# Performance work log

Hardware: AMD Instinct MI355X
Metric: run time of the kernel (lower is better)

## Reference

```python
import jax, jax.numpy as jnp
import numpy as np
from jax import lax

H = 1024
D = 128
T = 64  # n_step + n_middle


def gru_cell(x, h, w_ih, w_hh, b_ih, b_hh):
    # torch.nn.GRUCell gate order: r, z, n
    gi = x @ w_ih.T + b_ih
    gh = h @ w_hh.T + b_hh
    ir, iz, i_n = jnp.split(gi, 3, axis=-1)
    hr, hz, h_n = jnp.split(gh, 3, axis=-1)
    r = jax.nn.sigmoid(ir + hr)
    z = jax.nn.sigmoid(iz + hz)
    n = jnp.tanh(i_n + r * h_n)
    return (1.0 - z) * n + z * h


def decoder(z_seq, z8, n1, w_init, b_init, wi1, wh1, bi1, bh1, wi2, wh2, bi2, bh2, w_out, b_out):
    B = z_seq.shape[0]
    out0 = jnp.zeros((B, D), z_seq.dtype).at[:, -1].set(1.0)
    h0 = z8 @ w_init.T + b_init              # [B, H]
    h1 = jnp.zeros_like(h0)                  # replaced at i == 0
    xs = (jnp.arange(T), jnp.swapaxes(z_seq, 0, 1))  # ([T], [T, B, D])

    def step(carry, x):
        h0, h1, out = carry
        i, z_i = x
        inp = jnp.where(i <= n1 - 1, z_i, out)
        h0n = gru_cell(inp, h0, wi1, wh1, bi1, bh1)
        h1 = jnp.where(i == 0, h0n, h1)
        h1n = gru_cell(h0n, h1, wi2, wh2, bi2, bh2)
        out = h1n @ w_out.T + b_out          # [B, 128]
        return (h0n, h1n, out), out

    _, outs = lax.scan(step, (h0, h1, out0), xs)  # [T, B, 128]
    return jnp.swapaxes(outs[n1 - 1:], 0, 1)      # [B, T-n1+1, 128]


def _p(key, shape):
    return jax.random.normal(key, shape, dtype=jnp.float32) * 0.02


def setup_inputs() -> dict:
    key = jax.random.key(0)
    ks = jax.random.split(key, 32)
    B = 2048
    inp = {
        'zp': jax.random.normal(ks[0], (B, T, D), jnp.float32),
        'zr': jax.random.normal(ks[1], (B, T, D), jnp.float32),
        'zp8': jax.random.normal(ks[2], (B, D), jnp.float32),
        'zr8': jax.random.normal(ks[3], (B, D), jnp.float32),
        'n1': 16,
        'n2': 48,
    }
    # GRU cells 1..4: (w_ih [3H, in], w_hh [3H, H], b_ih [3H], b_hh [3H])
    for j, name in enumerate(['1', '2', '3', '4']):
        in_dim = D if name in ('1', '3') else H
        inp['wi' + name] = _p(ks[4 + 4 * j], (3 * H, in_dim))
        inp['wh' + name] = _p(ks[5 + 4 * j], (3 * H, H))
        inp['bi' + name] = _p(ks[6 + 4 * j], (3 * H,))
        inp['bh' + name] = _p(ks[7 + 4 * j], (3 * H,))
    inp['w_init0'] = _p(ks[20], (H, D)); inp['b_init0'] = _p(ks[21], (H,))
    inp['w_init1'] = _p(ks[22], (H, D)); inp['b_init1'] = _p(ks[23], (H,))
    inp['w_out0'] = _p(ks[24], (D, H)); inp['b_out0'] = _p(ks[25], (D,))
    inp['w_out1'] = _p(ks[26], (D, H)); inp['b_out1'] = _p(ks[27], (D,))
    return inp


def reference(zp, zr, zp8, zr8, n1, n2,
              wi1, wh1, bi1, bh1, wi2, wh2, bi2, bh2,
              wi3, wh3, bi3, bh3, wi4, wh4, bi4, bh4,
              w_init0, b_init0, w_init1, b_init1,
              w_out0, b_out0, w_out1, b_out1):
    z_r = decoder(zr, zr8, n1, w_init0, b_init0, wi1, wh1, bi1, bh1,
                  wi2, wh2, bi2, bh2, w_out0, b_out0)
    z_p = decoder(zp, zp8, n1, w_init1, b_init1, wi3, wh3, bi3, bh3,
                  wi4, wh4, bi4, bh4, w_out1, b_out1)
    return (z_p, z_r)
```

## Files before the change

kernel.cpp:

```cpp
#include <hip/hip_runtime.h>

typedef unsigned short u16;
typedef unsigned int u32;
typedef __attribute__((ext_vector_type(8))) short short8;
typedef __attribute__((ext_vector_type(4))) float f32x4;

#define DEV __device__ __forceinline__
#define SB0() __builtin_amdgcn_sched_barrier(0)

DEV u16 f2bf(float f){
  u32 u = __builtin_bit_cast(u32, f);
  u += 0x7fffu + ((u >> 16) & 1u);
  return (u16)(u >> 16);
}
DEV float sigm(float x){ return 1.f / (1.f + __expf(-x)); }
DEV float tanh_(float x){ return 2.f / (1.f + __expf(-2.f * x)) - 1.f; }

DEV void gl_lds16(const void* g, void* l){
  __builtin_amdgcn_global_load_lds(
      (const __attribute__((address_space(1))) u32*)g,
      (__attribute__((address_space(3))) u32*)l, 16, 0, 0);
}

#define MFMA16(A,B,C) __builtin_amdgcn_mfma_f32_16x16x32_bf16(A, B, C, 0, 0, 0)
#define LGKM0() do{ asm volatile("s_waitcnt lgkmcnt(0)" ::: "memory"); SB0(); }while(0)

__global__ void pack_w_kernel(const float* __restrict__ wi, const float* __restrict__ wh,
                              u16* __restrict__ dst, int Ki, int Kh, int nrows){
  const int KT = Ki + Kh;
  const long n = (long)nrows * KT;
  for (long idx = (long)blockIdx.x * blockDim.x + threadIdx.x; idx < n;
       idx += (long)gridDim.x * blockDim.x){
    int r = (int)(idx / KT), c = (int)(idx % KT);
    float v = (c < Ki) ? wi[(long)r * Ki + c] : wh[(long)r * Kh + (c - Ki)];
    dst[idx] = f2bf(v);
  }
}

struct InitA { const float* z8; const float* wini; const float* bini; float* h0f; u16* h0bf; };

__global__ __launch_bounds__(256)
void init_kernel(InitA A0, InitA A1){
  const InitA& a = (blockIdx.z == 0) ? A0 : A1;
  __shared__ float lz[64][128];
  const int tid = threadIdx.x;
  const int rb = blockIdx.x * 64, ub = blockIdx.y * 128;
  {
    const int row = tid >> 2, q = tid & 3;
    const float4* p = (const float4*)(a.z8 + (long)(rb + row) * 128 + q * 32);
    float4* dst = (float4*)&lz[row][q * 32];
    #pragma unroll
    for (int j = 0; j < 8; ++j) dst[j] = p[j];
  }
  __syncthreads();
  const int u = ub + (tid & 127);
  const int rg = tid >> 7;
  float acc[32];
  #pragma unroll
  for (int r = 0; r < 32; ++r) acc[r] = 0.f;
  for (int k = 0; k < 128; k += 4){
    float4 w4 = *(const float4*)&a.wini[(long)u * 128 + k];
    #pragma unroll
    for (int r = 0; r < 32; ++r){
      float4 z4 = *(const float4*)&lz[rg * 32 + r][k];
      acc[r] += w4.x * z4.x + w4.y * z4.y + w4.z * z4.z + w4.w * z4.w;
    }
  }
  const float b = a.bini[u];
  #pragma unroll
  for (int r = 0; r < 32; ++r){
    const long row = rb + rg * 32 + r;
    const float v = acc[r] + b;
    a.h0f[row * 1024 + u] = v;
    a.h0bf[row * 1024 + u] = f2bf(v);
  }
}

struct CellA {
  const u16* W;
  const float* bi; const float* bh;
  const float* afz; const float* afo;
  const u16* ab1; const u16* ab2;
  const float* holdr; float* holdw; u16* hbfw;
};

template<int CELL>
__global__ __attribute__((amdgpu_waves_per_eu(2, 2))) __launch_bounds__(512)
void cell_kernel(CellA A0, CellA A1, const int* dn1, int step){
  constexpr int KTOT = (CELL == 1) ? 1152 : 2048;
  constexpr int KT = KTOT / 64;
  constexpr int NI_STEPS = (CELL == 1) ? 2 : 16;

  __shared__ u16 lA[2][256 * 64];
  __shared__ u16 lB[2][192 * 64];

  const CellA& a = (blockIdx.y == 0) ? A0 : A1;
  const int tid = threadIdx.x;
  const int lane = tid & 63;
  const int wv = tid >> 6;
  const int wm = wv >> 1;
  const int wn = wv & 1;
  const int bid = blockIdx.x;
  const int inner = bid >> 3;
  const int m_idx = ((bid >> 2) & 1) * 4 + (inner & 3);
  const int n_idx = (bid & 3) * 4 + (inner >> 2);
  const int brow = m_idx * 256;
  const int u0 = n_idx * 64;

  f32x4 aR[4][2] = {}; f32x4 aZ[4][2] = {};
  f32x4 aNI[4][2] = {}; f32x4 aNH[4][2] = {};

  const int srow = tid >> 3;
  const int sxor8 = ((tid & 7) ^ (srow & 7)) * 8;

  auto stage = [&](int bf, int kt){
    const int k0 = kt * 64;
    const u16* ab; int kk;
    if constexpr (CELL == 1){ ab = a.ab1; kk = k0 - 128; }
    else { if (k0 < 1024){ ab = a.ab1; kk = k0; } else { ab = a.ab2; kk = k0 - 1024; } }
    #pragma unroll
    for (int j = 0; j < 4; ++j)
      gl_lds16(ab + (long)(brow + j * 64 + srow) * 1024 + kk + sxor8,
               &lA[bf][(j * 64 + wv * 8) * 64]);
    #pragma unroll
    for (int g = 0; g < 3; ++g)
      gl_lds16(a.W + (long)(g * 1024 + u0 + srow) * KTOT + k0 + sxor8,
               &lB[bf][(g * 64 + wv * 8) * 64]);
  };

  const int l15 = lane & 15;
  const int kq = lane >> 4;
  const int sx = lane & 7;

  auto read_a_ks = [&](int bf, int ks, short8 (&af)[4]){
    const int soff = (((ks * 4 + kq) ^ sx)) * 8;
    #pragma unroll
    for (int fr = 0; fr < 4; ++fr)
      af[fr] = *(const short8*)&lA[bf][(wm * 64 + fr * 16 + l15) * 64 + soff];
  };
  auto read_b_ks = [&](int bf, int g, int ks, short8 (&bg)[2]){
    const int soff = (((ks * 4 + kq) ^ sx)) * 8;
    #pragma unroll
    for (int fc = 0; fc < 2; ++fc)
      bg[fc] = *(const short8*)&lB[bf][(g * 64 + wn * 32 + fc * 16 + l15) * 64 + soff];
  };
  auto mfma8 = [&](const short8 (&af)[4], const short8 (&bg)[2], f32x4 (&A)[4][2]){
    #pragma unroll
    for (int fr = 0; fr < 4; ++fr)
      #pragma unroll
      for (int fc = 0; fc < 2; ++fc)
        A[fr][fc] = MFMA16(af[fr], bg[fc], A[fr][fc]);
  };

  int kstart;
  if constexpr (CELL == 1){
    const int n1v = *dn1;
    const float* fsrc; long fstr;
    if (step < n1v){ fsrc = a.afz; fstr = 64 * 128; }
    else           { fsrc = a.afo; fstr = 128; }
    {
      const int row = tid >> 1, half = tid & 1;
      #pragma unroll
      for (int st = 0; st < 2; ++st){
        const float* pp = fsrc + (long)(brow + row) * fstr + st * 64 + half * 32;
        #pragma unroll
        for (int q = 0; q < 4; ++q){
          float4 x = ((const float4*)pp)[2 * q];
          float4 y = ((const float4*)pp)[2 * q + 1];
          short8 o;
          o[0] = (short)f2bf(x.x); o[1] = (short)f2bf(x.y);
          o[2] = (short)f2bf(x.z); o[3] = (short)f2bf(x.w);
          o[4] = (short)f2bf(y.x); o[5] = (short)f2bf(y.y);
          o[6] = (short)f2bf(y.z); o[7] = (short)f2bf(y.w);
          const int s = half * 4 + q;
          *(short8*)&lA[st][row * 64 + ((s ^ (row & 7)) * 8)] = o;
        }
        #pragma unroll
        for (int g = 0; g < 3; ++g)
          gl_lds16(a.W + (long)(g * 1024 + u0 + srow) * KTOT + st * 64 + sxor8,
                   &lB[st][(g * 64 + wv * 8) * 64]);
      }
    }
    __syncthreads();
    #pragma unroll
    for (int st = 0; st < 2; ++st){
      short8 af0[4], af1[4], b0[2], b1[2];
      read_a_ks(st, 0, af0); read_a_ks(st, 1, af1);
      read_b_ks(st, 0, 0, b0); read_b_ks(st, 0, 1, b1);
      LGKM0();
      mfma8(af0, b0, aR); mfma8(af1, b1, aR);
      read_b_ks(st, 1, 0, b0); read_b_ks(st, 1, 1, b1);
      LGKM0();
      mfma8(af0, b0, aZ); mfma8(af1, b1, aZ);
      read_b_ks(st, 2, 0, b0); read_b_ks(st, 2, 1, b1);
      LGKM0();
      mfma8(af0, b0, aNI); mfma8(af1, b1, aNI);
    }
    __syncthreads();
    stage(0, 2); stage(1, 3);
    asm volatile("s_waitcnt vmcnt(7)" ::: "memory"); SB0();
    __builtin_amdgcn_s_barrier();
    kstart = 2;
  } else {
    stage(0, 0); stage(1, 1);
    asm volatile("s_waitcnt vmcnt(7)" ::: "memory"); SB0();
    __builtin_amdgcn_s_barrier();
    kstart = 0;
  }

  for (int kt = kstart; kt < KT; ++kt){
    const int b = kt & 1;
    short8 af0[4], af1[4], bR0[2], bR1[2], bZ0[2], bZ1[2], bN0[2], bN1[2];
    read_a_ks(b, 0, af0); read_b_ks(b, 0, 0, bR0); read_b_ks(b, 1, 0, bZ0);
    __builtin_amdgcn_s_barrier();
    LGKM0();
    __builtin_amdgcn_s_setprio(1);
    mfma8(af0, bR0, aR);
    __builtin_amdgcn_s_setprio(0);
    __builtin_amdgcn_s_barrier(); SB0();
    read_b_ks(b, 2, 0, bN0); read_a_ks(b, 1, af1);
    __builtin_amdgcn_s_barrier();
    LGKM0();
    __builtin_amdgcn_s_setprio(1);
    mfma8(af0, bZ0, aZ);
    if (kt < NI_STEPS) mfma8(af0, bN0, aNI); else mfma8(af0, bN0, aNH);
    __builtin_amdgcn_s_setprio(0);
    __builtin_amdgcn_s_barrier(); SB0();
    read_b_ks(b, 0, 1, bR1); read_b_ks(b, 1, 1, bZ1); read_b_ks(b, 2, 1, bN1);
    __builtin_amdgcn_s_barrier();
    LGKM0();
    __builtin_amdgcn_s_setprio(1);
    mfma8(af1, bR1, aR);
    __builtin_amdgcn_s_setprio(0);
    __builtin_amdgcn_s_barrier(); SB0();
    if (kt + 2 < KT) stage(b, kt + 2);
    __builtin_amdgcn_s_setprio(1);
    mfma8(af1, bZ1, aZ);
    if (kt < NI_STEPS) mfma8(af1, bN1, aNI); else mfma8(af1, bN1, aNH);
    __builtin_amdgcn_s_setprio(0);
    if (kt < KT - 2)       { asm volatile("s_waitcnt vmcnt(7)" ::: "memory"); SB0(); }
    else if (kt == KT - 2) { asm volatile("s_waitcnt vmcnt(0)" ::: "memory"); SB0(); }
    if (kt + 1 < KT) __builtin_amdgcn_s_barrier();
  }

  const int rq = (lane >> 4) * 4;
  #pragma unroll
  for (int fc = 0; fc < 2; ++fc){
    const int u = u0 + wn * 32 + fc * 16 + l15;
    const float br = a.bi[u] + a.bh[u];
    const float bz = a.bi[1024 + u] + a.bh[1024 + u];
    const float bni = a.bi[2048 + u];
    const float bnh = a.bh[2048 + u];
    #pragma unroll
    for (int fr = 0; fr < 4; ++fr){
      #pragma unroll
      for (int rg = 0; rg < 4; ++rg){
        const long row = brow + wm * 64 + fr * 16 + rq + rg;
        const float r = sigm(aR[fr][fc][rg] + br);
        const float z = sigm(aZ[fr][fc][rg] + bz);
        const float n = tanh_(aNI[fr][fc][rg] + bni + r * (aNH[fr][fc][rg] + bnh));
        const float hp = a.holdr[row * 1024 + u];
        const float hn = (1.f - z) * n + z * hp;
        a.holdw[row * 1024 + u] = hn;
        a.hbfw[row * 1024 + u] = f2bf(hn);
      }
    }
  }
}

struct OutA { const u16* Ah; const u16* Wo; const float* bo; float* outf; };

__global__ __launch_bounds__(256, 2)
void out_kernel(OutA A0, OutA A1, const int* dn1, int step, float* __restrict__ dout, long outhalf){
  const int n1v = *dn1;
  if (step < n1v - 1) return;
  __shared__ u16 lA[2][32 * 64];
  __shared__ u16 lB[2][128 * 64];
  const OutA& a = (blockIdx.y == 0) ? A0 : A1;
  const int tid = threadIdx.x, lane = tid & 63, wv = tid >> 6;
  const int brow = blockIdx.x * 32;
  f32x4 acc[2][2] = {};
  const int srow = tid >> 3;
  const int sxor8 = ((tid & 7) ^ (srow & 7)) * 8;

  auto stage = [&](int bf, int kt){
    const int k0 = kt * 64;
    gl_lds16(a.Ah + (long)(brow + srow) * 1024 + k0 + sxor8, &lA[bf][wv * 8 * 64]);
    #pragma unroll
    for (int j = 0; j < 4; ++j)
      gl_lds16(a.Wo + (long)(j * 32 + srow) * 1024 + k0 + sxor8,
               &lB[bf][(j * 32 + wv * 8) * 64]);
  };

  stage(0, 0); stage(1, 1);
  const int l15 = lane & 15, kq = lane >> 4, sx = lane & 7;
  for (int kt = 0; kt < 16; ++kt){
    const int b = kt & 1;
    if (kt < 15) asm volatile("s_waitcnt vmcnt(5)" ::: "memory");
    else         asm volatile("s_waitcnt vmcnt(0)" ::: "memory");
    SB0();
    __builtin_amdgcn_s_barrier();
    SB0();
    short8 af[2][2], bf2[2][2];
    #pragma unroll
    for (int ks = 0; ks < 2; ++ks){
      const int soff = (((ks * 4 + kq) ^ sx)) * 8;
      af[ks][0] = *(const short8*)&lA[b][(l15) * 64 + soff];
      af[ks][1] = *(const short8*)&lA[b][(16 + l15) * 64 + soff];
      bf2[ks][0] = *(const short8*)&lB[b][(wv * 32 + l15) * 64 + soff];
      bf2[ks][1] = *(const short8*)&lB[b][(wv * 32 + 16 + l15) * 64 + soff];
    }
    asm volatile("s_waitcnt lgkmcnt(0)" ::: "memory"); SB0();
    __builtin_amdgcn_s_barrier();
    SB0();
    if (kt + 2 < 16) stage(b, kt + 2);
    __builtin_amdgcn_s_setprio(1);
    #pragma unroll
    for (int ks = 0; ks < 2; ++ks)
      #pragma unroll
      for (int fr = 0; fr < 2; ++fr)
        #pragma unroll
        for (int fc = 0; fc < 2; ++fc)
          acc[fr][fc] = MFMA16(af[ks][fr], bf2[ks][fc], acc[fr][fc]);
    __builtin_amdgcn_s_setprio(0);
  }
  const int nst = 65 - n1v;
  const int t = step - (n1v - 1);
  const int rq = (lane >> 4) * 4;
  #pragma unroll
  for (int fc = 0; fc < 2; ++fc){
    const int u = wv * 32 + fc * 16 + l15;
    const float bo = a.bo[u];
    #pragma unroll
    for (int fr = 0; fr < 2; ++fr){
      #pragma unroll
      for (int rg = 0; rg < 4; ++rg){
        const long row = brow + fr * 16 + rq + rg;
        const float v = acc[fr][fc][rg] + bo;
        a.outf[row * 128 + u] = v;
        dout[(long)blockIdx.y * outhalf + (row * nst + t) * 128 + u] = v;
      }
    }
  }
}

extern "C" void kernel_launch(void* const* d_in, const int* in_sizes, int n_in,
                              void* d_out, int out_size, void* d_ws, size_t ws_size,
                              hipStream_t stream){
  const float* zz[2]   = { (const float*)d_in[0],  (const float*)d_in[1] };
  const float* z8[2]   = { (const float*)d_in[2],  (const float*)d_in[3] };
  const int* dn1       = (const int*)d_in[4];
  const float* wi_c1[2] = { (const float*)d_in[14], (const float*)d_in[6] };
  const float* wh_c1[2] = { (const float*)d_in[15], (const float*)d_in[7] };
  const float* bi_c1[2] = { (const float*)d_in[16], (const float*)d_in[8] };
  const float* bh_c1[2] = { (const float*)d_in[17], (const float*)d_in[9] };
  const float* wi_c2[2] = { (const float*)d_in[18], (const float*)d_in[10] };
  const float* wh_c2[2] = { (const float*)d_in[19], (const float*)d_in[11] };
  const float* bi_c2[2] = { (const float*)d_in[20], (const float*)d_in[12] };
  const float* bh_c2[2] = { (const float*)d_in[21], (const float*)d_in[13] };
  const float* wini[2]  = { (const float*)d_in[24], (const float*)d_in[22] };
  const float* bini[2]  = { (const float*)d_in[25], (const float*)d_in[23] };
  const float* wout[2]  = { (const float*)d_in[28], (const float*)d_in[26] };
  const float* bout[2]  = { (const float*)d_in[29], (const float*)d_in[27] };

  char* p = (char*)d_ws;
  auto alloc = [&](size_t bytes)->char*{
    char* q = p; p += (bytes + 255) & ~(size_t)255; return q;
  };
  u16* W1c[2]; u16* W2c[2]; u16* Woc[2];
  float* h0f[2]; float* h1f[2]; float* outf[2];
  u16* h0bf[2][2]; u16* h1bf[2][2];
  for (int d = 0; d < 2; ++d){
    W1c[d] = (u16*)alloc(3072ULL * 1152 * 2);
    W2c[d] = (u16*)alloc(3072ULL * 2048 * 2);
    Woc[d] = (u16*)alloc(128ULL * 1024 * 2);
    h0f[d] = (float*)alloc(2048ULL * 1024 * 4);
    h1f[d] = (float*)alloc(2048ULL * 1024 * 4);
    outf[d] = (float*)alloc(2048ULL * 128 * 4);
    for (int b = 0; b < 2; ++b){
      h0bf[d][b] = (u16*)alloc(2048ULL * 1024 * 2);
      h1bf[d][b] = (u16*)alloc(2048ULL * 1024 * 2);
    }
  }
  if ((size_t)(p - (char*)d_ws) > ws_size) return;

  for (int d = 0; d < 2; ++d){
    pack_w_kernel<<<dim3(1024), dim3(256), 0, stream>>>(wi_c1[d], wh_c1[d], W1c[d], 128, 1024, 3072);
    pack_w_kernel<<<dim3(1024), dim3(256), 0, stream>>>(wi_c2[d], wh_c2[d], W2c[d], 1024, 1024, 3072);
    pack_w_kernel<<<dim3(64),   dim3(256), 0, stream>>>(wout[d], wout[d], Woc[d], 1024, 0, 128);
  }
  {
    InitA I0{ z8[0], wini[0], bini[0], h0f[0], h0bf[0][0] };
    InitA I1{ z8[1], wini[1], bini[1], h0f[1], h0bf[1][0] };
    init_kernel<<<dim3(32, 8, 2), dim3(256), 0, stream>>>(I0, I1);
  }

  const long outhalf = (long)out_size / 2;

  for (int i = 0; i < 64; ++i){
    const int cur = i & 1, nxt = cur ^ 1;
    CellA c1[2], c2[2];
    for (int d = 0; d < 2; ++d){
      c1[d] = CellA{ W1c[d], bi_c1[d], bh_c1[d],
                     zz[d] + (long)i * 128, outf[d],
                     h0bf[d][cur], nullptr,
                     h0f[d], h0f[d], h0bf[d][nxt] };
      c2[d] = CellA{ W2c[d], bi_c2[d], bh_c2[d],
                     nullptr, nullptr,
                     h0bf[d][nxt], (i == 0) ? h0bf[d][nxt] : h1bf[d][cur],
                     (i == 0) ? h0f[d] : h1f[d], h1f[d], h1bf[d][nxt] };
    }
    cell_kernel<1><<<dim3(128, 2), dim3(512), 0, stream>>>(c1[0], c1[1], dn1, i);
    cell_kernel<2><<<dim3(128, 2), dim3(512), 0, stream>>>(c2[0], c2[1], dn1, i);
    OutA o0{ h1bf[0][nxt], Woc[0], bout[0], outf[0] };
    OutA o1{ h1bf[1][nxt], Woc[1], bout[1], outf[1] };
    out_kernel<<<dim3(64, 2), dim3(256), 0, stream>>>(o0, o1, dn1, i, (float*)d_out, outhalf);
  }
}
```

Measured before the change: 7.355 ms.

## Regroup GRU GEMM phases by row-fragment pairs and split A/B staging

Measured after the change: 7.210 ms. 2.0% less time.

```diff
diff --git a/kernel.cpp b/kernel.cpp
--- a/kernel.cpp
+++ b/kernel.cpp
@@ -24,6 +24,7 @@
 
 #define MFMA16(A,B,C) __builtin_amdgcn_mfma_f32_16x16x32_bf16(A, B, C, 0, 0, 0)
 #define LGKM0() do{ asm volatile("s_waitcnt lgkmcnt(0)" ::: "memory"); SB0(); }while(0)
+#define BAR()  do{ __builtin_amdgcn_s_barrier(); SB0(); }while(0)
 
 __global__ void pack_w_kernel(const float* __restrict__ wi, const float* __restrict__ wh,
                               u16* __restrict__ dst, int Ki, int Kh, int nrows){
@@ -113,7 +114,7 @@
   const int srow = tid >> 3;
   const int sxor8 = ((tid & 7) ^ (srow & 7)) * 8;
 
-  auto stage = [&](int bf, int kt){
+  auto stageA = [&](int bf, int kt){
     const int k0 = kt * 64;
     const u16* ab; int kk;
     if constexpr (CELL == 1){ ab = a.ab1; kk = k0 - 128; }
@@ -122,6 +123,9 @@
     for (int j = 0; j < 4; ++j)
       gl_lds16(ab + (long)(brow + j * 64 + srow) * 1024 + kk + sxor8,
                &lA[bf][(j * 64 + wv * 8) * 64]);
+  };
+  auto stageB = [&](int bf, int kt){
+    const int k0 = kt * 64;
     #pragma unroll
     for (int g = 0; g < 3; ++g)
       gl_lds16(a.W + (long)(g * 1024 + u0 + srow) * KTOT + k0 + sxor8,
@@ -132,24 +136,32 @@
   const int kq = lane >> 4;
   const int sx = lane & 7;
 
-  auto read_a_ks = [&](int bf, int ks, short8 (&af)[4]){
+  auto read_a2 = [&](int bf, int ks, int rbh, short8 (&af)[2]){
     const int soff = (((ks * 4 + kq) ^ sx)) * 8;
     #pragma unroll
-    for (int fr = 0; fr < 4; ++fr)
-      af[fr] = *(const short8*)&lA[bf][(wm * 64 + fr * 16 + l15) * 64 + soff];
-  };
-  auto read_b_ks = [&](int bf, int g, int ks, short8 (&bg)[2]){
+    for (int i = 0; i < 2; ++i)
+      af[i] = *(const short8*)&lA[bf][(wm * 64 + (rbh * 2 + i) * 16 + l15) * 64 + soff];
+  };
+  auto read_b6 = [&](int bf, int ks, short8 (&bg)[6]){
     const int soff = (((ks * 4 + kq) ^ sx)) * 8;
     #pragma unroll
-    for (int fc = 0; fc < 2; ++fc)
-      bg[fc] = *(const short8*)&lB[bf][(g * 64 + wn * 32 + fc * 16 + l15) * 64 + soff];
-  };
-  auto mfma8 = [&](const short8 (&af)[4], const short8 (&bg)[2], f32x4 (&A)[4][2]){
-    #pragma unroll
-    for (int fr = 0; fr < 4; ++fr)
+    for (int g = 0; g < 3; ++g)
       #pragma unroll
       for (int fc = 0; fc < 2; ++fc)
-        A[fr][fc] = MFMA16(af[fr], bg[fc], A[fr][fc]);
+        bg[g * 2 + fc] = *(const short8*)&lB[bf][(g * 64 + wn * 32 + fc * 16 + l15) * 64 + soff];
+  };
+  auto mfma12 = [&](const short8 (&af)[2], int fr0, const short8 (&bg)[6], bool toNI){
+    #pragma unroll
+    for (int i = 0; i < 2; ++i){
+      const int fr = fr0 + i;
+      #pragma unroll
+      for (int fc = 0; fc < 2; ++fc){
+        aR[fr][fc] = MFMA16(af[i], bg[fc], aR[fr][fc]);
+        aZ[fr][fc] = MFMA16(af[i], bg[2 + fc], aZ[fr][fc]);
+        if (toNI) aNI[fr][fc] = MFMA16(af[i], bg[4 + fc], aNI[fr][fc]);
+        else      aNH[fr][fc] = MFMA16(af[i], bg[4 + fc], aNH[fr][fc]);
+      }
+    }
   };
 
   int kstart;
@@ -175,72 +187,66 @@
           const int s = half * 4 + q;
           *(short8*)&lA[st][row * 64 + ((s ^ (row & 7)) * 8)] = o;
         }
-        #pragma unroll
-        for (int g = 0; g < 3; ++g)
-          gl_lds16(a.W + (long)(g * 1024 + u0 + srow) * KTOT + st * 64 + sxor8,
-                   &lB[st][(g * 64 + wv * 8) * 64]);
+        stageB(st, st);
       }
     }
     __syncthreads();
     #pragma unroll
     for (int st = 0; st < 2; ++st){
-      short8 af0[4], af1[4], b0[2], b1[2];
-      read_a_ks(st, 0, af0); read_a_ks(st, 1, af1);
-      read_b_ks(st, 0, 0, b0); read_b_ks(st, 0, 1, b1);
-      LGKM0();
-      mfma8(af0, b0, aR); mfma8(af1, b1, aR);
-      read_b_ks(st, 1, 0, b0); read_b_ks(st, 1, 1, b1);
-      LGKM0();
-      mfma8(af0, b0, aZ); mfma8(af1, b1, aZ);
-      read_b_ks(st, 2, 0, b0); read_b_ks(st, 2, 1, b1);
-      LGKM0();
-      mfma8(af0, b0, aNI); mfma8(af1, b1, aNI);
+      #pragma unroll
+      for (int ks = 0; ks < 2; ++ks){
+        short8 a01[2], a23[2], bgh[6];
+        read_a2(st, ks, 0, a01); read_a2(st, ks, 1, a23); read_b6(st, ks, bgh);
+        LGKM0();
+        mfma12(a01, 0, bgh, true);
+        mfma12(a23, 2, bgh, true);
+      }
     }
     __syncthreads();
-    stage(0, 2); stage(1, 3);
+    stageA(0, 2); stageB(0, 2); stageA(1, 3); stageB(1, 3);
     asm volatile("s_waitcnt vmcnt(7)" ::: "memory"); SB0();
-    __builtin_amdgcn_s_barrier();
+    BAR();
     kstart = 2;
   } else {
-    stage(0, 0); stage(1, 1);
+    stageA(0, 0); stageB(0, 0); stageA(1, 1); stageB(1, 1);
     asm volatile("s_waitcnt vmcnt(7)" ::: "memory"); SB0();
-    __builtin_amdgcn_s_barrier();
+    BAR();
     kstart = 0;
   }
 
   for (int kt = kstart; kt < KT; ++kt){
     const int b = kt & 1;
-    short8 af0[4], af1[4], bR0[2], bR1[2], bZ0[2], bZ1[2], bN0[2], bN1[2];
-    read_a_ks(b, 0, af0); read_b_ks(b, 0, 0, bR0); read_b_ks(b, 1, 0, bZ0);
-    __builtin_amdgcn_s_barrier();
+    const bool toNI = (kt < NI_STEPS);
+    short8 a01k0[2], a01k1[2], a23k0[2], a23k1[2], bg0[6], bg1[6];
+    read_a2(b, 0, 0, a01k0); read_a2(b, 1, 0, a01k1); read_b6(b, 0, bg0); SB0();
+    BAR();
     LGKM0();
     __builtin_amdgcn_s_setprio(1);
-    mfma8(af0, bR0, aR);
+    mfma12(a01k0, 0, bg0, toNI);
     __builtin_amdgcn_s_setprio(0);
-    __builtin_amdgcn_s_barrier(); SB0();
-    read_b_ks(b, 2, 0, bN0); read_a_ks(b, 1, af1);
-    __builtin_amdgcn_s_barrier();
+    BAR();
+    read_a2(b, 0, 1, a23k0); read_a2(b, 1, 1, a23k1); SB0();
+    BAR();
     LGKM0();
     __builtin_amdgcn_s_setprio(1);
-    mfma8(af0, bZ0, aZ);
-    if (kt < NI_STEPS) mfma8(af0, bN0, aNI); else mfma8(af0, bN0, aNH);
+    mfma12(a23k0, 2, bg0, toNI);
     __builtin_amdgcn_s_setprio(0);
-    __builtin_amdgcn_s_barrier(); SB0();
-    read_b_ks(b, 0, 1, bR1); read_b_ks(b, 1, 1, bZ1); read_b_ks(b, 2, 1, bN1);
-    __builtin_amdgcn_s_barrier();
+    BAR();
+    read_b6(b, 1, bg1); SB0();
+    if (kt + 2 < KT) stageA(b, kt + 2);
+    BAR();
     LGKM0();
     __builtin_amdgcn_s_setprio(1);
-    mfma8(af1, bR1, aR);
+    mfma12(a01k1, 0, bg1, toNI);
     __builtin_amdgcn_s_setprio(0);
-    __builtin_amdgcn_s_barrier(); SB0();
-    if (kt + 2 < KT) stage(b, kt + 2);
+    BAR();
+    if (kt + 2 < KT) stageB(b, kt + 2);
     __builtin_amdgcn_s_setprio(1);
-    mfma8(af1, bZ1, aZ);
-    if (kt < NI_STEPS) mfma8(af1, bN1, aNI); else mfma8(af1, bN1, aNH);
+    mfma12(a23k1, 2, bg1, toNI);
     __builtin_amdgcn_s_setprio(0);
     if (kt < KT - 2)       { asm volatile("s_waitcnt vmcnt(7)" ::: "memory"); SB0(); }
     else if (kt == KT - 2) { asm volatile("s_waitcnt vmcnt(0)" ::: "memory"); SB0(); }
-    if (kt + 1 < KT) __builtin_amdgcn_s_barrier();
+    if (kt + 1 < KT) BAR();
   }
 
   const int rq = (lane >> 4) * 4;
```
